# Optimization experiments

Measured on AMD Instinct MI355X. Metric: run time of the kernel, lower is better.

## Reference

```python
import jax, jax.numpy as jnp
import numpy as np
from jax import lax

B, T, CD, HD, VD, QD = 2048, 20, 512, 1024, 2048, 1024

def leaky(x):
    return jax.nn.leaky_relu(x, negative_slope=0.01)

def gru_cell(x, h, w_ih, w_hh, b_ih, b_hh):
    # torch.nn.GRUCell math
    gi = x @ w_ih.T + b_ih            # [B, 3H]
    gh = h @ w_hh.T + b_hh            # [B, 3H]
    i_r, i_z, i_n = jnp.split(gi, 3, axis=-1)
    h_r, h_z, h_n = jnp.split(gh, 3, axis=-1)
    r = jax.nn.sigmoid(i_r + h_r)
    z = jax.nn.sigmoid(i_z + h_z)
    n = jnp.tanh(i_n + r * h_n)
    return (1.0 - z) * n + z * h


def setup_inputs() -> dict:
    key = jax.random.key(0)
    ks = jax.random.split(key, 16)
    s = 0.05
    return {
        "v": jax.random.normal(ks[0], (B, VD), dtype=jnp.float32),
        "q": jax.random.normal(ks[1], (B, QD), dtype=jnp.float32),
        "caption": jax.random.normal(ks[2], (B, T, CD), dtype=jnp.float32),
        "cap_len": jax.random.randint(ks[3], (B,), 0, T),
        # word_rnn: GRUCell(c_dim -> c_dim)
        "w_ih1": jax.random.normal(ks[4], (3 * CD, CD), dtype=jnp.float32) * s,
        "w_hh1": jax.random.normal(ks[5], (3 * CD, CD), dtype=jnp.float32) * s,
        "b_ih1": jax.random.normal(ks[6], (3 * CD,), dtype=jnp.float32) * s,
        "b_hh1": jax.random.normal(ks[7], (3 * CD,), dtype=jnp.float32) * s,
        # caption_rnn: GRUCell(c_dim -> hidden_dim)
        "w_ih2": jax.random.normal(ks[8], (3 * HD, CD), dtype=jnp.float32) * s,
        "w_hh2": jax.random.normal(ks[9], (3 * HD, HD), dtype=jnp.float32) * s,
        "b_ih2": jax.random.normal(ks[10], (3 * HD,), dtype=jnp.float32) * s,
        "b_hh2": jax.random.normal(ks[11], (3 * HD,), dtype=jnp.float32) * s,
        # attention: W_v Linear(v_dim -> c_dim, no bias), W_q Linear(q_dim -> c_dim, no bias)
        "Wv": jax.random.normal(ks[12], (CD, VD), dtype=jnp.float32) * s,
        "Wq": jax.random.normal(ks[13], (CD, QD), dtype=jnp.float32) * s,
        # fcnet: Linear(hidden_dim -> hidden_dim, no bias)
        "Wfc": jax.random.normal(ks[14], (HD, HD), dtype=jnp.float32) * s,
    }


def reference(v, q, caption, cap_len, w_ih1, w_hh1, b_ih1, b_hh1,
              w_ih2, w_hh2, b_ih2, b_hh2, Wv, Wq, Wfc):
    # Dropout is inference-mode identity. Sorting by length + restore_id is
    # equivalent to full-batch masked processing in original order.
    b = caption.shape[0]
    fv = leaky(v @ Wv.T)              # [B, c_dim] attention visual projection
    fq = leaky(q @ Wq.T)              # [B, c_dim]
    cap_t = jnp.transpose(caption, (1, 0, 2))  # [T, B, c_dim]

    h1_0 = jnp.zeros((b, CD), caption.dtype)
    h2_0 = jnp.zeros((b, HD), caption.dtype)

    def step(carry, inputs):
        h1, h2 = carry
        x_t, t = inputs
        active = (t < cap_len)[:, None]           # rows still inside their caption
        h1n = gru_cell(x_t, h1, w_ih1, w_hh1, b_ih1, b_hh1)
        h1 = jnp.where(active, h1n, h1)
        att = jax.nn.sigmoid(h1 * fv + h1 * fq) * x_t   # [B, c_dim]
        h2n = gru_cell(att, h2, w_ih2, w_hh2, b_ih2, b_hh2)
        h2 = jnp.where(active, h2n, h2)
        out_t = jnp.where(active, leaky(h2 @ Wfc.T), 0.0)  # [B, hidden]
        a_t = jnp.where(active, att, 0.0)                  # [B, c_dim]
        return (h1, h2), (out_t, a_t)

    (_, _), (outs, alphas) = lax.scan(step, (h1_0, h2_0),
                                      (cap_t, jnp.arange(T)))
    # MaxPool1d over the time axis of [B, hidden, T] (zeros at padded steps)
    output = jnp.max(outs, axis=0)               # [B, hidden]
    alphas = jnp.transpose(alphas, (1, 0, 2))    # [B, T, c_dim]
    return output, alphas
```

## Files before the change

kernel.cpp:

```cpp
#include <hip/hip_runtime.h>

typedef _Float16 half_t;
typedef half_t half8 __attribute__((ext_vector_type(8)));
typedef half_t half4 __attribute__((ext_vector_type(4)));
typedef float  floatx4 __attribute__((ext_vector_type(4)));

#define NB 2048
#define NT 20
#define CD 512
#define HD 1024
#define VD 2048
#define QD 1024


__device__ __forceinline__ float sigmoidf_(float x) { return 1.0f / (1.0f + __expf(-x)); }
__device__ __forceinline__ float tanhf_(float x)    { return 1.0f - 2.0f / (1.0f + __expf(2.0f * x)); }
__device__ __forceinline__ float lrelu_(float x)    { return x > 0.0f ? x : 0.01f * x; }

__device__ __forceinline__ void gload16(const half_t* g, half_t* l) {
    __builtin_amdgcn_global_load_lds(
        (const __attribute__((address_space(1))) void*)g,
        (__attribute__((address_space(3))) void*)l, 16, 0, 0);
}

__device__ __forceinline__ void remap(int flat, int GX, int& m0, int& c0) {
    const int xcd = flat & 7;
    const int i   = flat >> 3;
    c0 = (xcd * (GX >> 3) + (i >> 4)) * 32;
    m0 = (i & 15) * 128;
}

template <int NG, int NACC,
          int I0A, int I1A, int I2A, int I0B, int I1B, int I2B>
__device__ __forceinline__ void gemm2(
    const half_t* __restrict__ A1, int lda1, const half_t* __restrict__ W1, long gs1, int S1,
    const half_t* __restrict__ A2, int lda2, const half_t* __restrict__ W2, long gs2, int S2,
    int m0, int c0, half_t* lds, floatx4 (&acc)[NACC][2][1])
{
    constexpr int ASZ = 128 * 64;
    constexpr int WCH = NG * 256;
    constexpr int BUF = ASZ + NG * 2048;
    constexpr int map_[3] = {I0A, I1A, I2A};
    constexpr int mapB[3] = {I0B, I1B, I2B};

    const int tid  = threadIdx.x;
    const int lane = tid & 63;
    const int wid  = tid >> 6;
    const int wr   = (wid >> 1) * 32;
    const int wc   = (wid & 1) * 16;
    const int frow = lane & 15;
    const int cb   = lane >> 4;

    const int arow = tid >> 3;
    const int aq   = ((tid & 7) ^ (arow & 7)) * 8;
    const int adst = arow * 64 + (tid & 7) * 8;
    const long aof1 = (long)(m0 + arow) * lda1 + aq;
    const long aof2 = (long)(m0 + arow) * lda2 + aq;

    const bool w0v = tid < WCH;
    const bool w1v = tid + 512 < WCH;
    int wdst0, wdst1; long wof10, wof11, wof20, wof21;
    {
        const int u = tid;
        const int g = u >> 8, idx = u & 255, row = idx >> 3, ch = idx & 7;
        const int q = (ch ^ (row & 7)) * 8;
        wdst0 = ASZ + u * 8;
        wof10 = (long)g * gs1 + (long)(c0 + row) * (S1 * 64) + q;
        wof20 = (long)g * gs2 + (long)(c0 + row) * (S2 * 64) + q;
    }
    {
        const int u = tid + 512;
        const int g = u >> 8, idx = u & 255, row = idx >> 3, ch = idx & 7;
        const int q = (ch ^ (row & 7)) * 8;
        wdst1 = ASZ + u * 8;
        wof11 = (long)g * gs1 + (long)(c0 + row) * (S1 * 64) + q;
        wof21 = (long)g * gs2 + (long)(c0 + row) * (S2 * 64) + q;
    }

    const int S = S1 + S2;
    auto stage = [&](int s, int buf) {
        half_t* lb = lds + buf * BUF;
        if (s < S1) {
            const int k0 = s * 64;
            gload16(A1 + aof1 + k0,             lb + adst);
            gload16(A1 + aof1 + 64 * lda1 + k0, lb + adst + 64 * 64);
            if (w0v) gload16(W1 + wof10 + k0, lb + wdst0);
            if (w1v) gload16(W1 + wof11 + k0, lb + wdst1);
        } else {
            const int k0 = (s - S1) * 64;
            gload16(A2 + aof2 + k0,             lb + adst);
            gload16(A2 + aof2 + 64 * lda2 + k0, lb + adst + 64 * 64);
            if (w0v) gload16(W2 + wof20 + k0, lb + wdst0);
            if (w1v) gload16(W2 + wof21 + k0, lb + wdst1);
        }
    };

    stage(0, 0);
    __syncthreads();
    int cur = 0;
    for (int s = 0; s < S; ++s) {
        if (s + 1 < S) stage(s + 1, cur ^ 1);
        const half_t* lb = lds + cur * BUF;
        const bool pa = (s < S1);
#pragma unroll
        for (int kk = 0; kk < 2; ++kk) {
            half8 af[2];
#pragma unroll
            for (int im = 0; im < 2; ++im) {
                const int r = wr + im * 16 + frow;
                af[im] = *(const half8*)(lb + r * 64 + (((kk * 4 + cb) ^ (r & 7)) * 8));
            }
#pragma unroll
            for (int g = 0; g < NG; ++g) {
                const int r = wc + frow;
                const half8 bf = *(const half8*)(lb + ASZ + g * 2048 + r * 64 +
                                                 (((kk * 4 + cb) ^ (r & 7)) * 8));
                const int d = pa ? map_[g] : mapB[g];
#pragma unroll
                for (int im = 0; im < 2; ++im)
                    acc[d][im][0] = __builtin_amdgcn_mfma_f32_16x16x32_f16(
                        af[im], bf, acc[d][im][0], 0, 0, 0);
            }
        }
        __syncthreads();
        cur ^= 1;
    }
}

__global__ void sort_kernel(const int* __restrict__ cap_len,
                            int* __restrict__ perm, int* __restrict__ cnt)
{
    __shared__ int hist[NT];
    __shared__ int off[NT];
    const int tid = threadIdx.x;
    if (tid < NT) hist[tid] = 0;
    __syncthreads();
    for (int i = tid; i < NB; i += 256) atomicAdd(&hist[cap_len[i]], 1);
    __syncthreads();
    if (tid == 0) {
        int run = 0;
        for (int v = NT - 1; v >= 0; --v) { off[v] = run; run += hist[v]; }
        for (int t = 0; t < NT; ++t) cnt[t] = off[t];
        for (int t = NT; t < 32; ++t) cnt[t] = 0;
    }
    __syncthreads();
    for (int i = tid; i < NB; i += 256) {
        const int pos = atomicAdd(&off[cap_len[i]], 1);
        perm[pos] = i;
    }
}

struct CvtArgs {
    const float* src[10];
    half_t* dst[10];
    int start[11];
    int rowlen[10];
    const int* perm;
    const int* cnt;
};
__global__ void cvt_all_kernel(CvtArgs a) {
    const int b = blockIdx.x;
    int i = 0;
#pragma unroll
    for (int k = 0; k < 9; ++k) i += (b >= a.start[k + 1]);
    const int idx = ((b - a.start[i]) * 256 + (int)threadIdx.x) * 4;
    long sidx = idx;
    const int rl = a.rowlen[i];
    if (rl) {
        const int row = idx / rl;
        if (row >= a.cnt[0]) return;
        sidx = (long)a.perm[row] * rl + (idx - row * rl);
    }
    float4 f = *(const float4*)(a.src[i] + sidx);
    half4 h = {(half_t)f.x, (half_t)f.y, (half_t)f.z, (half_t)f.w};
    *(half4*)(a.dst[i] + idx) = h;
}


__device__ __forceinline__ void step1_body(
    int flat,
    const half_t* __restrict__ cap_h,
    const half_t* __restrict__ wih1, const half_t* __restrict__ whh1,
    const float* __restrict__ b_ih1, const float* __restrict__ b_hh1,
    const half_t* __restrict__ h1_src, half_t* __restrict__ h1_dst,
    const float* __restrict__ fvq, const float* __restrict__ caption,
    const int* __restrict__ perm, int cn,
    half_t* __restrict__ att_w, float* __restrict__ alphas, int t, half_t* lds)
{
    int m0, c0; remap(flat, 16, m0, c0);
    if (m0 >= cn) return;
    floatx4 acc[4][2][1];
#pragma unroll
    for (int g = 0; g < 4; ++g) for (int im = 0; im < 2; ++im)
        acc[g][im][0] = (floatx4){0.f, 0.f, 0.f, 0.f};
    gemm2<3, 4, 0, 1, 2, 0, 1, 3>(
        cap_h + t * CD, NT * CD, wih1, (long)CD * CD, CD / 64,
        h1_src, CD, whh1, (long)CD * CD, CD / 64, m0, c0, lds, acc);

    const int lane = threadIdx.x & 63;
    const int wid = threadIdx.x >> 6;
    const int wr = (wid >> 1) * 32, wc = (wid & 1) * 16;
#pragma unroll
    for (int im = 0; im < 2; ++im) {
        const int mb = m0 + wr + im * 16 + (lane >> 4) * 4;
        const int c  = c0 + wc + (lane & 15);
        const float br = b_ih1[c] + b_hh1[c];
        const float bz = b_ih1[CD + c] + b_hh1[CD + c];
        const float bin_ = b_ih1[2 * CD + c];
        const float bhn  = b_hh1[2 * CD + c];
#pragma unroll
        for (int j = 0; j < 4; ++j) {
            const int m = mb + j;
            const float r = sigmoidf_(acc[0][im][0][j] + br);
            const float z = sigmoidf_(acc[1][im][0][j] + bz);
            const float n = tanhf_(acc[2][im][0][j] + bin_ + r * (acc[3][im][0][j] + bhn));
            const float h_old = (float)h1_src[m * CD + c];
            const bool act = m < cn;
            const float h_new = act ? ((1.f - z) * n + z * h_old) : h_old;
            const int orig = perm[m];
            const float x = caption[((long)orig * NT + t) * CD + c];
            const float at = sigmoidf_(h_new * fvq[m * CD + c]) * x;
            h1_dst[m * CD + c] = (half_t)h_new;
            att_w[m * CD + c]  = (half_t)at;
            if (act) alphas[((long)orig * NT + t) * CD + c] = at;
        }
    }
}

__device__ __forceinline__ void step2_body(
    int flat,
    const half_t* __restrict__ att_r,
    const half_t* __restrict__ wih2, const half_t* __restrict__ whh2,
    const float* __restrict__ b_ih2, const float* __restrict__ b_hh2,
    const half_t* __restrict__ h2_src, half_t* __restrict__ h2_dst,
    int cn, int t, half_t* lds)
{
    int m0, c0; remap(flat, 32, m0, c0);
    if (m0 >= cn) return;
    floatx4 acc[4][2][1];
#pragma unroll
    for (int g = 0; g < 4; ++g) for (int im = 0; im < 2; ++im)
        acc[g][im][0] = (floatx4){0.f, 0.f, 0.f, 0.f};
    gemm2<3, 4, 0, 1, 2, 0, 1, 3>(
        att_r, CD, wih2, (long)HD * CD, CD / 64,
        h2_src, HD, whh2, (long)HD * HD, HD / 64, m0, c0, lds, acc);

    const int lane = threadIdx.x & 63;
    const int wid = threadIdx.x >> 6;
    const int wr = (wid >> 1) * 32, wc = (wid & 1) * 16;
#pragma unroll
    for (int im = 0; im < 2; ++im) {
        const int mb = m0 + wr + im * 16 + (lane >> 4) * 4;
        const int c  = c0 + wc + (lane & 15);
        const float br = b_ih2[c] + b_hh2[c];
        const float bz = b_ih2[HD + c] + b_hh2[HD + c];
        const float bin_ = b_ih2[2 * HD + c];
        const float bhn  = b_hh2[2 * HD + c];
#pragma unroll
        for (int j = 0; j < 4; ++j) {
            const int m = mb + j;
            const float r = sigmoidf_(acc[0][im][0][j] + br);
            const float z = sigmoidf_(acc[1][im][0][j] + bz);
            const float n = tanhf_(acc[2][im][0][j] + bin_ + r * (acc[3][im][0][j] + bhn));
            const float h_old = (float)h2_src[m * HD + c];
            const bool act = m < cn;
            h2_dst[m * HD + c] = (half_t)(act ? ((1.f - z) * n + z * h_old) : h_old);
        }
    }
}

__device__ __forceinline__ void step3_body(
    int flat,
    const half_t* __restrict__ h2_cur, const half_t* __restrict__ wfc,
    const int* __restrict__ perm, int cn,
    float* __restrict__ outmax, half_t* lds)
{
    int m0, c0; remap(flat, 32, m0, c0);
    if (m0 >= cn) return;
    floatx4 acc[1][2][1];
#pragma unroll
    for (int im = 0; im < 2; ++im)
        acc[0][im][0] = (floatx4){0.f, 0.f, 0.f, 0.f};
    gemm2<1, 1, 0, 0, 0, 0, 0, 0>(
        h2_cur, HD, wfc, 0, HD / 64,
        h2_cur, HD, wfc, 0, 0, m0, c0, lds, acc);

    const int lane = threadIdx.x & 63;
    const int wid = threadIdx.x >> 6;
    const int wr = (wid >> 1) * 32, wc = (wid & 1) * 16;
#pragma unroll
    for (int im = 0; im < 2; ++im) {
        const int mb = m0 + wr + im * 16 + (lane >> 4) * 4;
        const int c  = c0 + wc + (lane & 15);
#pragma unroll
        for (int j = 0; j < 4; ++j) {
            const int m = mb + j;
            if (m < cn) {
                const int orig = perm[m];
                const float v0 = lrelu_(acc[0][im][0][j]);
                float* p = &outmax[(long)orig * HD + c];
                *p = fmaxf(*p, v0);
            }
        }
    }
}

__global__ __launch_bounds__(512, 4) void step1_0_kernel(
    const half_t* __restrict__ v_h, const half_t* __restrict__ wv_w,
    const half_t* __restrict__ q_h, const half_t* __restrict__ wq_w,
    const half_t* __restrict__ cap_h, const half_t* __restrict__ wih1,
    const float* __restrict__ b_ih1, const float* __restrict__ b_hh1,
    half_t* __restrict__ h1_dst, float* __restrict__ fvq_out,
    const float* __restrict__ caption, const int* __restrict__ perm,
    const int* __restrict__ cnt,
    half_t* __restrict__ att_w, float* __restrict__ alphas)
{
    __shared__ half_t lds[2 * (128 * 64 + 3 * 2048)];
    const int cn = cnt[0];
    int m0, c0; remap(blockIdx.x, 16, m0, c0);
    if (m0 >= cn) return;

    floatx4 acc1[2][2][1];
#pragma unroll
    for (int g = 0; g < 2; ++g) for (int im = 0; im < 2; ++im)
        acc1[g][im][0] = (floatx4){0.f, 0.f, 0.f, 0.f};
    gemm2<1, 2, 0, 0, 0, 1, 0, 0>(
        v_h, VD, wv_w, 0, VD / 64, q_h, QD, wq_w, 0, QD / 64, m0, c0, lds, acc1);

    floatx4 acc2[3][2][1];
#pragma unroll
    for (int g = 0; g < 3; ++g) for (int im = 0; im < 2; ++im)
        acc2[g][im][0] = (floatx4){0.f, 0.f, 0.f, 0.f};
    gemm2<3, 3, 0, 1, 2, 0, 1, 2>(
        cap_h, NT * CD, wih1, (long)CD * CD, CD / 64,
        cap_h, NT * CD, wih1, (long)CD * CD, 0, m0, c0, lds, acc2);

    const int lane = threadIdx.x & 63;
    const int wid = threadIdx.x >> 6;
    const int wr = (wid >> 1) * 32, wc = (wid & 1) * 16;
#pragma unroll
    for (int im = 0; im < 2; ++im) {
        const int mb = m0 + wr + im * 16 + (lane >> 4) * 4;
        const int c  = c0 + wc + (lane & 15);
        const float br = b_ih1[c] + b_hh1[c];
        const float bz = b_ih1[CD + c] + b_hh1[CD + c];
        const float bin_ = b_ih1[2 * CD + c];
        const float bhn  = b_hh1[2 * CD + c];
#pragma unroll
        for (int j = 0; j < 4; ++j) {
            const int m = mb + j;
            const float fv = lrelu_(acc1[0][im][0][j]) + lrelu_(acc1[1][im][0][j]);
            fvq_out[m * CD + c] = fv;
            const float r = sigmoidf_(acc2[0][im][0][j] + br);
            const float z = sigmoidf_(acc2[1][im][0][j] + bz);
            const float n = tanhf_(acc2[2][im][0][j] + bin_ + r * bhn);
            const bool act = m < cn;
            const float h_new = act ? (1.f - z) * n : 0.f;
            const int orig = perm[m];
            const float x = caption[(long)orig * NT * CD + c];
            const float at = sigmoidf_(h_new * fv) * x;
            h1_dst[m * CD + c] = (half_t)h_new;
            att_w[m * CD + c]  = (half_t)at;
            if (act) alphas[(long)orig * NT * CD + c] = at;
        }
    }
}

__global__ __launch_bounds__(512, 4) void fused321_kernel(
    const half_t* __restrict__ att0, half_t* __restrict__ att1,
    const half_t* __restrict__ wih2, const half_t* __restrict__ whh2,
    const float* __restrict__ b_ih2, const float* __restrict__ b_hh2,
    const half_t* __restrict__ h2b0, half_t* __restrict__ h2b1,
    const half_t* __restrict__ cap_h,
    const half_t* __restrict__ wih1, const half_t* __restrict__ whh1,
    const float* __restrict__ b_ih1, const float* __restrict__ b_hh1,
    const half_t* __restrict__ h1b0, half_t* __restrict__ h1b1,
    const float* __restrict__ fvq, const float* __restrict__ caption,
    const half_t* __restrict__ wfc,
    const int* __restrict__ perm, const int* __restrict__ cnt,
    float* __restrict__ outmax, float* __restrict__ alphas, int t)
{
    __shared__ half_t lds[2 * (128 * 64 + 3 * 2048)];
    const int par = t & 1;
    const half_t* att_r = par ? att1 : att0;
    half_t*       att_w = par ? (half_t*)att0 : att1;
    const half_t* h2_r  = par ? h2b1 : h2b0;
    half_t*       h2_w  = par ? (half_t*)h2b0 : h2b1;
    const half_t* h1_r  = par ? h1b0 : h1b1;
    half_t*       h1_w  = par ? h1b1 : (half_t*)h1b0;

    const int bx = blockIdx.x;
    if (bx < 512) {
        if (t < NT)
            step2_body(bx, att_r, wih2, whh2, b_ih2, b_hh2, h2_r, h2_w,
                       cnt[t], t, lds);
    } else if (bx < 768) {
        if (t < NT - 1)
            step1_body(bx - 512, cap_h, wih1, whh1, b_ih1, b_hh1,
                       h1_r, h1_w, fvq, caption, perm, cnt[t + 1],
                       att_w, alphas, t + 1, lds);
    } else {
        if (t >= 1)
            step3_body(bx - 768, h2_r, wfc, perm, cnt[t - 1], outmax, lds);
    }
}

extern "C" void kernel_launch(void* const* d_in, const int* in_sizes, int n_in,
                              void* d_out, int out_size, void* d_ws, size_t ws_size,
                              hipStream_t stream)
{
    (void)in_sizes; (void)n_in; (void)out_size; (void)ws_size;
    const float* v     = (const float*)d_in[0];
    const float* q     = (const float*)d_in[1];
    const float* cap   = (const float*)d_in[2];
    const int*   cap_len = (const int*)d_in[3];
    const float* w_ih1 = (const float*)d_in[4];
    const float* w_hh1 = (const float*)d_in[5];
    const float* b_ih1 = (const float*)d_in[6];
    const float* b_hh1 = (const float*)d_in[7];
    const float* w_ih2 = (const float*)d_in[8];
    const float* w_hh2 = (const float*)d_in[9];
    const float* b_ih2 = (const float*)d_in[10];
    const float* b_hh2 = (const float*)d_in[11];
    const float* Wv    = (const float*)d_in[12];
    const float* Wq    = (const float*)d_in[13];
    const float* Wfc   = (const float*)d_in[14];

    float* out_max = (float*)d_out;
    float* alphas  = (float*)d_out + (size_t)NB * HD;

    half_t* p = (half_t*)d_ws;
    half_t* v_h    = p; p += (size_t)NB * VD;
    half_t* q_h    = p; p += (size_t)NB * QD;
    half_t* cap_h  = p; p += (size_t)NB * NT * CD;
    half_t* wih1_h = p; p += 3 * CD * CD;
    half_t* whh1_h = p; p += 3 * CD * CD;
    half_t* wih2_h = p; p += 3 * HD * CD;
    half_t* whh2_h = p; p += 3 * HD * HD;
    half_t* wfc_h  = p; p += HD * HD;
    half_t* wv_h   = p; p += CD * VD;
    half_t* wq_h   = p; p += CD * QD;
    half_t* h1b0   = p; p += (size_t)NB * CD;
    half_t* h1b1   = p; p += (size_t)NB * CD;
    half_t* h2b0   = p; p += (size_t)NB * HD;
    half_t* h2b1   = p; p += (size_t)NB * HD;
    half_t* att0   = p; p += (size_t)NB * CD;
    half_t* att1   = p; p += (size_t)NB * CD;
    float* fvq = (float*)p; p += (size_t)NB * CD * 2;
    int* perm = (int*)p;
    int* cnt  = perm + NB;

    hipMemsetAsync(out_max, 0, (size_t)NB * HD * sizeof(float), stream);
    hipMemsetAsync(alphas, 0, (size_t)NB * NT * CD * sizeof(float), stream);
    hipMemsetAsync(h2b0, 0, (size_t)NB * HD * sizeof(half_t), stream);

    sort_kernel<<<1, 256, 0, stream>>>(cap_len, perm, cnt);

    CvtArgs ca;
    const float* srcs[10] = {v, q, cap, w_ih1, w_hh1, w_ih2, w_hh2, Wfc, Wv, Wq};
    half_t* dsts[10] = {v_h, q_h, cap_h, wih1_h, whh1_h, wih2_h, whh2_h, wfc_h, wv_h, wq_h};
    const int ns[10] = {NB * VD, NB * QD, NB * NT * CD, 3 * CD * CD, 3 * CD * CD,
                        3 * HD * CD, 3 * HD * HD, HD * HD, CD * VD, CD * QD};
    const int rls[10] = {VD, QD, NT * CD, 0, 0, 0, 0, 0, 0, 0};
    int acc_blk = 0;
    for (int i = 0; i < 10; ++i) {
        ca.src[i] = srcs[i]; ca.dst[i] = dsts[i]; ca.rowlen[i] = rls[i];
        ca.start[i] = acc_blk; acc_blk += ns[i] / 1024;
    }
    ca.start[10] = acc_blk;
    ca.perm = perm; ca.cnt = cnt;
    cvt_all_kernel<<<acc_blk, 256, 0, stream>>>(ca);

    step1_0_kernel<<<256, 512, 0, stream>>>(
        v_h, wv_h, q_h, wq_h, cap_h, wih1_h, b_ih1, b_hh1,
        h1b1, fvq, cap, perm, cnt, att0, alphas);

    for (int t = 0; t <= NT; ++t) {
        fused321_kernel<<<1280, 512, 0, stream>>>(
            att0, att1, wih2_h, whh2_h, b_ih2, b_hh2, h2b0, h2b1,
            cap_h, wih1_h, whh1_h, b_ih1, b_hh1, h1b0, h1b1,
            fvq, cap, wfc_h, perm, cnt, out_max, alphas, t);
    }
}
```

Measured before the change: 973.9 us.

## Widen GEMM output tile from 32 to 64 columns per block

```diff
diff --git a/kernel.cpp b/kernel.cpp
--- a/kernel.cpp
+++ b/kernel.cpp
@@ -26,7 +26,7 @@
 __device__ __forceinline__ void remap(int flat, int GX, int& m0, int& c0) {
     const int xcd = flat & 7;
     const int i   = flat >> 3;
-    c0 = (xcd * (GX >> 3) + (i >> 4)) * 32;
+    c0 = (xcd * (GX >> 3) + (i >> 4)) * 64;
     m0 = (i & 15) * 128;
 }
 
@@ -35,11 +35,10 @@
 __device__ __forceinline__ void gemm2(
     const half_t* __restrict__ A1, int lda1, const half_t* __restrict__ W1, long gs1, int S1,
     const half_t* __restrict__ A2, int lda2, const half_t* __restrict__ W2, long gs2, int S2,
-    int m0, int c0, half_t* lds, floatx4 (&acc)[NACC][2][1])
+    int m0, int c0, half_t* lds, floatx4 (&acc)[NACC][2][2])
 {
     constexpr int ASZ = 128 * 64;
-    constexpr int WCH = NG * 256;
-    constexpr int BUF = ASZ + NG * 2048;
+    constexpr int BUF = ASZ + NG * 4096;
     constexpr int map_[3] = {I0A, I1A, I2A};
     constexpr int mapB[3] = {I0B, I1B, I2B};
 
@@ -47,34 +46,30 @@
     const int lane = tid & 63;
     const int wid  = tid >> 6;
     const int wr   = (wid >> 1) * 32;
-    const int wc   = (wid & 1) * 16;
+    const int wc   = (wid & 1) * 32;
     const int frow = lane & 15;
     const int cb   = lane >> 4;
 
-    const int arow = tid >> 3;
-    const int aq   = ((tid & 7) ^ (arow & 7)) * 8;
-    const int adst = arow * 64 + (tid & 7) * 8;
-    const long aof1 = (long)(m0 + arow) * lda1 + aq;
-    const long aof2 = (long)(m0 + arow) * lda2 + aq;
-
-    const bool w0v = tid < WCH;
-    const bool w1v = tid + 512 < WCH;
-    int wdst0, wdst1; long wof10, wof11, wof20, wof21;
-    {
-        const int u = tid;
-        const int g = u >> 8, idx = u & 255, row = idx >> 3, ch = idx & 7;
+    long aof1[2], aof2[2]; int adst[2];
+#pragma unroll
+    for (int j = 0; j < 2; ++j) {
+        const int u = tid + j * 512;
+        const int row = u >> 3, ch = u & 7;
         const int q = (ch ^ (row & 7)) * 8;
-        wdst0 = ASZ + u * 8;
-        wof10 = (long)g * gs1 + (long)(c0 + row) * (S1 * 64) + q;
-        wof20 = (long)g * gs2 + (long)(c0 + row) * (S2 * 64) + q;
-    }
-    {
-        const int u = tid + 512;
-        const int g = u >> 8, idx = u & 255, row = idx >> 3, ch = idx & 7;
+        adst[j] = u * 8;
+        aof1[j] = (long)(m0 + row) * lda1 + q;
+        aof2[j] = (long)(m0 + row) * lda2 + q;
+    }
+    long wof1[NG], wof2[NG]; int wdst[NG];
+#pragma unroll
+    for (int j = 0; j < NG; ++j) {
+        const int u = tid + j * 512;
+        const int g = u >> 9, idx = u & 511;
+        const int row = idx >> 3, ch = idx & 7;
         const int q = (ch ^ (row & 7)) * 8;
-        wdst1 = ASZ + u * 8;
-        wof11 = (long)g * gs1 + (long)(c0 + row) * (S1 * 64) + q;
-        wof21 = (long)g * gs2 + (long)(c0 + row) * (S2 * 64) + q;
+        wdst[j] = ASZ + u * 8;
+        wof1[j] = (long)g * gs1 + (long)(c0 + row) * (S1 * 64) + q;
+        wof2[j] = (long)g * gs2 + (long)(c0 + row) * (S2 * 64) + q;
     }
 
     const int S = S1 + S2;
@@ -82,16 +77,16 @@
         half_t* lb = lds + buf * BUF;
         if (s < S1) {
             const int k0 = s * 64;
-            gload16(A1 + aof1 + k0,             lb + adst);
-            gload16(A1 + aof1 + 64 * lda1 + k0, lb + adst + 64 * 64);
-            if (w0v) gload16(W1 + wof10 + k0, lb + wdst0);
-            if (w1v) gload16(W1 + wof11 + k0, lb + wdst1);
+#pragma unroll
+            for (int j = 0; j < 2; ++j)  gload16(A1 + aof1[j] + k0, lb + adst[j]);
+#pragma unroll
+            for (int j = 0; j < NG; ++j) gload16(W1 + wof1[j] + k0, lb + wdst[j]);
         } else {
             const int k0 = (s - S1) * 64;
-            gload16(A2 + aof2 + k0,             lb + adst);
-            gload16(A2 + aof2 + 64 * lda2 + k0, lb + adst + 64 * 64);
-            if (w0v) gload16(W2 + wof20 + k0, lb + wdst0);
-            if (w1v) gload16(W2 + wof21 + k0, lb + wdst1);
+#pragma unroll
+            for (int j = 0; j < 2; ++j)  gload16(A2 + aof2[j] + k0, lb + adst[j]);
+#pragma unroll
+            for (int j = 0; j < NG; ++j) gload16(W2 + wof2[j] + k0, lb + wdst[j]);
         }
     };
 
@@ -112,14 +107,17 @@
             }
 #pragma unroll
             for (int g = 0; g < NG; ++g) {
-                const int r = wc + frow;
-                const half8 bf = *(const half8*)(lb + ASZ + g * 2048 + r * 64 +
-                                                 (((kk * 4 + cb) ^ (r & 7)) * 8));
-                const int d = pa ? map_[g] : mapB[g];
-#pragma unroll
-                for (int im = 0; im < 2; ++im)
-                    acc[d][im][0] = __builtin_amdgcn_mfma_f32_16x16x32_f16(
-                        af[im], bf, acc[d][im][0], 0, 0, 0);
+#pragma unroll
+                for (int in = 0; in < 2; ++in) {
+                    const int r = wc + in * 16 + frow;
+                    const half8 bf = *(const half8*)(lb + ASZ + g * 4096 + r * 64 +
+                                                     (((kk * 4 + cb) ^ (r & 7)) * 8));
+                    const int d = pa ? map_[g] : mapB[g];
+#pragma unroll
+                    for (int im = 0; im < 2; ++im)
+                        acc[d][im][in] = __builtin_amdgcn_mfma_f32_16x16x32_f16(
+                            af[im], bf, acc[d][im][in], 0, 0, 0);
+                }
             }
         }
         __syncthreads();
@@ -187,23 +185,25 @@
     const int* __restrict__ perm, int cn,
     half_t* __restrict__ att_w, float* __restrict__ alphas, int t, half_t* lds)
 {
-    int m0, c0; remap(flat, 16, m0, c0);
+    int m0, c0; remap(flat, 8, m0, c0);
     if (m0 >= cn) return;
-    floatx4 acc[4][2][1];
-#pragma unroll
-    for (int g = 0; g < 4; ++g) for (int im = 0; im < 2; ++im)
-        acc[g][im][0] = (floatx4){0.f, 0.f, 0.f, 0.f};
+    floatx4 acc[4][2][2];
+#pragma unroll
+    for (int g = 0; g < 4; ++g) for (int im = 0; im < 2; ++im) for (int in = 0; in < 2; ++in)
+        acc[g][im][in] = (floatx4){0.f, 0.f, 0.f, 0.f};
     gemm2<3, 4, 0, 1, 2, 0, 1, 3>(
         cap_h + t * CD, NT * CD, wih1, (long)CD * CD, CD / 64,
         h1_src, CD, whh1, (long)CD * CD, CD / 64, m0, c0, lds, acc);
 
     const int lane = threadIdx.x & 63;
     const int wid = threadIdx.x >> 6;
-    const int wr = (wid >> 1) * 32, wc = (wid & 1) * 16;
-#pragma unroll
-    for (int im = 0; im < 2; ++im) {
+    const int wr = (wid >> 1) * 32, wc = (wid & 1) * 32;
+#pragma unroll
+    for (int im = 0; im < 2; ++im)
+#pragma unroll
+    for (int in = 0; in < 2; ++in) {
         const int mb = m0 + wr + im * 16 + (lane >> 4) * 4;
-        const int c  = c0 + wc + (lane & 15);
+        const int c  = c0 + wc + in * 16 + (lane & 15);
         const float br = b_ih1[c] + b_hh1[c];
         const float bz = b_ih1[CD + c] + b_hh1[CD + c];
         const float bin_ = b_ih1[2 * CD + c];
@@ -211,9 +211,9 @@
 #pragma unroll
         for (int j = 0; j < 4; ++j) {
             const int m = mb + j;
-            const float r = sigmoidf_(acc[0][im][0][j] + br);
-            const float z = sigmoidf_(acc[1][im][0][j] + bz);
-            const float n = tanhf_(acc[2][im][0][j] + bin_ + r * (acc[3][im][0][j] + bhn));
+            const float r = sigmoidf_(acc[0][im][in][j] + br);
+            const float z = sigmoidf_(acc[1][im][in][j] + bz);
+            const float n = tanhf_(acc[2][im][in][j] + bin_ + r * (acc[3][im][in][j] + bhn));
             const float h_old = (float)h1_src[m * CD + c];
             const bool act = m < cn;
             const float h_new = act ? ((1.f - z) * n + z * h_old) : h_old;
@@ -235,23 +235,25 @@
     const half_t* __restrict__ h2_src, half_t* __restrict__ h2_dst,
     int cn, int t, half_t* lds)
 {
-    int m0, c0; remap(flat, 32, m0, c0);
+    int m0, c0; remap(flat, 16, m0, c0);
     if (m0 >= cn) return;
-    floatx4 acc[4][2][1];
-#pragma unroll
-    for (int g = 0; g < 4; ++g) for (int im = 0; im < 2; ++im)
-        acc[g][im][0] = (floatx4){0.f, 0.f, 0.f, 0.f};
+    floatx4 acc[4][2][2];
+#pragma unroll
+    for (int g = 0; g < 4; ++g) for (int im = 0; im < 2; ++im) for (int in = 0; in < 2; ++in)
+        acc[g][im][in] = (floatx4){0.f, 0.f, 0.f, 0.f};
     gemm2<3, 4, 0, 1, 2, 0, 1, 3>(
         att_r, CD, wih2, (long)HD * CD, CD / 64,
         h2_src, HD, whh2, (long)HD * HD, HD / 64, m0, c0, lds, acc);
 
     const int lane = threadIdx.x & 63;
     const int wid = threadIdx.x >> 6;
-    const int wr = (wid >> 1) * 32, wc = (wid & 1) * 16;
-#pragma unroll
-    for (int im = 0; im < 2; ++im) {
+    const int wr = (wid >> 1) * 32, wc = (wid & 1) * 32;
+#pragma unroll
+    for (int im = 0; im < 2; ++im)
+#pragma unroll
+    for (int in = 0; in < 2; ++in) {
         const int mb = m0 + wr + im * 16 + (lane >> 4) * 4;
-        const int c  = c0 + wc + (lane & 15);
+        const int c  = c0 + wc + in * 16 + (lane & 15);
         const float br = b_ih2[c] + b_hh2[c];
         const float bz = b_ih2[HD + c] + b_hh2[HD + c];
         const float bin_ = b_ih2[2 * HD + c];
@@ -259,9 +261,9 @@
 #pragma unroll
         for (int j = 0; j < 4; ++j) {
             const int m = mb + j;
-            const float r = sigmoidf_(acc[0][im][0][j] + br);
-            const float z = sigmoidf_(acc[1][im][0][j] + bz);
-            const float n = tanhf_(acc[2][im][0][j] + bin_ + r * (acc[3][im][0][j] + bhn));
+            const float r = sigmoidf_(acc[0][im][in][j] + br);
+            const float z = sigmoidf_(acc[1][im][in][j] + bz);
+            const float n = tanhf_(acc[2][im][in][j] + bin_ + r * (acc[3][im][in][j] + bhn));
             const float h_old = (float)h2_src[m * HD + c];
             const bool act = m < cn;
             h2_dst[m * HD + c] = (half_t)(act ? ((1.f - z) * n + z * h_old) : h_old);
@@ -275,29 +277,31 @@
     const int* __restrict__ perm, int cn,
     float* __restrict__ outmax, half_t* lds)
 {
-    int m0, c0; remap(flat, 32, m0, c0);
+    int m0, c0; remap(flat, 16, m0, c0);
     if (m0 >= cn) return;
-    floatx4 acc[1][2][1];
-#pragma unroll
-    for (int im = 0; im < 2; ++im)
-        acc[0][im][0] = (floatx4){0.f, 0.f, 0.f, 0.f};
+    floatx4 acc[1][2][2];
+#pragma unroll
+    for (int im = 0; im < 2; ++im) for (int in = 0; in < 2; ++in)
+        acc[0][im][in] = (floatx4){0.f, 0.f, 0.f, 0.f};
     gemm2<1, 1, 0, 0, 0, 0, 0, 0>(
         h2_cur, HD, wfc, 0, HD / 64,
         h2_cur, HD, wfc, 0, 0, m0, c0, lds, acc);
 
     const int lane = threadIdx.x & 63;
     const int wid = threadIdx.x >> 6;
-    const int wr = (wid >> 1) * 32, wc = (wid & 1) * 16;
-#pragma unroll
-    for (int im = 0; im < 2; ++im) {
+    const int wr = (wid >> 1) * 32, wc = (wid & 1) * 32;
+#pragma unroll
+    for (int im = 0; im < 2; ++im)
+#pragma unroll
+    for (int in = 0; in < 2; ++in) {
         const int mb = m0 + wr + im * 16 + (lane >> 4) * 4;
-        const int c  = c0 + wc + (lane & 15);
+        const int c  = c0 + wc + in * 16 + (lane & 15);
 #pragma unroll
         for (int j = 0; j < 4; ++j) {
             const int m = mb + j;
             if (m < cn) {
                 const int orig = perm[m];
-                const float v0 = lrelu_(acc[0][im][0][j]);
+                const float v0 = lrelu_(acc[0][im][in][j]);
                 float* p = &outmax[(long)orig * HD + c];
                 *p = fmaxf(*p, v0);
             }
@@ -305,7 +309,7 @@
     }
 }
 
-__global__ __launch_bounds__(512, 4) void step1_0_kernel(
+__global__ __launch_bounds__(512, 2) void step1_0_kernel(
     const half_t* __restrict__ v_h, const half_t* __restrict__ wv_w,
     const half_t* __restrict__ q_h, const half_t* __restrict__ wq_w,
     const half_t* __restrict__ cap_h, const half_t* __restrict__ wih1,
@@ -315,33 +319,35 @@
     const int* __restrict__ cnt,
     half_t* __restrict__ att_w, float* __restrict__ alphas)
 {
-    __shared__ half_t lds[2 * (128 * 64 + 3 * 2048)];
+    __shared__ half_t lds[2 * (128 * 64 + 3 * 4096)];
     const int cn = cnt[0];
-    int m0, c0; remap(blockIdx.x, 16, m0, c0);
+    int m0, c0; remap(blockIdx.x, 8, m0, c0);
     if (m0 >= cn) return;
 
-    floatx4 acc1[2][2][1];
-#pragma unroll
-    for (int g = 0; g < 2; ++g) for (int im = 0; im < 2; ++im)
-        acc1[g][im][0] = (floatx4){0.f, 0.f, 0.f, 0.f};
+    floatx4 acc1[2][2][2];
+#pragma unroll
+    for (int g = 0; g < 2; ++g) for (int im = 0; im < 2; ++im) for (int in = 0; in < 2; ++in)
+        acc1[g][im][in] = (floatx4){0.f, 0.f, 0.f, 0.f};
     gemm2<1, 2, 0, 0, 0, 1, 0, 0>(
         v_h, VD, wv_w, 0, VD / 64, q_h, QD, wq_w, 0, QD / 64, m0, c0, lds, acc1);
 
-    floatx4 acc2[3][2][1];
-#pragma unroll
-    for (int g = 0; g < 3; ++g) for (int im = 0; im < 2; ++im)
-        acc2[g][im][0] = (floatx4){0.f, 0.f, 0.f, 0.f};
+    floatx4 acc2[3][2][2];
+#pragma unroll
+    for (int g = 0; g < 3; ++g) for (int im = 0; im < 2; ++im) for (int in = 0; in < 2; ++in)
+        acc2[g][im][in] = (floatx4){0.f, 0.f, 0.f, 0.f};
     gemm2<3, 3, 0, 1, 2, 0, 1, 2>(
         cap_h, NT * CD, wih1, (long)CD * CD, CD / 64,
         cap_h, NT * CD, wih1, (long)CD * CD, 0, m0, c0, lds, acc2);
 
     const int lane = threadIdx.x & 63;
     const int wid = threadIdx.x >> 6;
-    const int wr = (wid >> 1) * 32, wc = (wid & 1) * 16;
-#pragma unroll
-    for (int im = 0; im < 2; ++im) {
+    const int wr = (wid >> 1) * 32, wc = (wid & 1) * 32;
+#pragma unroll
+    for (int im = 0; im < 2; ++im)
+#pragma unroll
+    for (int in = 0; in < 2; ++in) {
         const int mb = m0 + wr + im * 16 + (lane >> 4) * 4;
-        const int c  = c0 + wc + (lane & 15);
+        const int c  = c0 + wc + in * 16 + (lane & 15);
         const float br = b_ih1[c] + b_hh1[c];
         const float bz = b_ih1[CD + c] + b_hh1[CD + c];
         const float bin_ = b_ih1[2 * CD + c];
@@ -349,11 +355,11 @@
 #pragma unroll
         for (int j = 0; j < 4; ++j) {
             const int m = mb + j;
-            const float fv = lrelu_(acc1[0][im][0][j]) + lrelu_(acc1[1][im][0][j]);
+            const float fv = lrelu_(acc1[0][im][in][j]) + lrelu_(acc1[1][im][in][j]);
             fvq_out[m * CD + c] = fv;
-            const float r = sigmoidf_(acc2[0][im][0][j] + br);
-            const float z = sigmoidf_(acc2[1][im][0][j] + bz);
-            const float n = tanhf_(acc2[2][im][0][j] + bin_ + r * bhn);
+            const float r = sigmoidf_(acc2[0][im][in][j] + br);
+            const float z = sigmoidf_(acc2[1][im][in][j] + bz);
+            const float n = tanhf_(acc2[2][im][in][j] + bin_ + r * bhn);
             const bool act = m < cn;
             const float h_new = act ? (1.f - z) * n : 0.f;
             const int orig = perm[m];
@@ -380,7 +386,7 @@
     const int* __restrict__ perm, const int* __restrict__ cnt,
     float* __restrict__ outmax, float* __restrict__ alphas, int t)
 {
-    __shared__ half_t lds[2 * (128 * 64 + 3 * 2048)];
+    __shared__ half_t lds[2 * (128 * 64 + 3 * 4096)];
     const int par = t & 1;
     const half_t* att_r = par ? att1 : att0;
     half_t*       att_w = par ? (half_t*)att0 : att1;
@@ -390,18 +396,18 @@
     half_t*       h1_w  = par ? h1b1 : (half_t*)h1b0;
 
     const int bx = blockIdx.x;
-    if (bx < 512) {
+    if (bx < 256) {
         if (t < NT)
             step2_body(bx, att_r, wih2, whh2, b_ih2, b_hh2, h2_r, h2_w,
                        cnt[t], t, lds);
-    } else if (bx < 768) {
+    } else if (bx < 512) {
+        if (t >= 1)
+            step3_body(bx - 256, h2_r, wfc, perm, cnt[t - 1], outmax, lds);
+    } else {
         if (t < NT - 1)
             step1_body(bx - 512, cap_h, wih1, whh1, b_ih1, b_hh1,
                        h1_r, h1_w, fvq, caption, perm, cnt[t + 1],
                        att_w, alphas, t + 1, lds);
-    } else {
-        if (t >= 1)
-            step3_body(bx - 768, h2_r, wfc, perm, cnt[t - 1], outmax, lds);
     }
 }
 
@@ -471,12 +477,12 @@
     ca.perm = perm; ca.cnt = cnt;
     cvt_all_kernel<<<acc_blk, 256, 0, stream>>>(ca);
 
-    step1_0_kernel<<<256, 512, 0, stream>>>(
+    step1_0_kernel<<<128, 512, 0, stream>>>(
         v_h, wv_h, q_h, wq_h, cap_h, wih1_h, b_ih1, b_hh1,
         h1b1, fvq, cap, perm, cnt, att0, alphas);
 
     for (int t = 0; t <= NT; ++t) {
-        fused321_kernel<<<1280, 512, 0, stream>>>(
+        fused321_kernel<<<640, 512, 0, stream>>>(
             att0, att1, wih2_h, whh2_h, b_ih2, b_hh2, h2b0, h2b1,
             cap_h, wih1_h, whh1_h, b_ih1, b_hh1, h1b0, h1b1,
             fvq, cap, wfc_h, perm, cnt, out_max, alphas, t);
```

New measurement: 983.2 us. Within noise of the previous version (+1.0%).
